# Performance work log

Measured on AMD Instinct MI355X. Metric: run time of the kernel, lower is better.

## Reference

```python
import jax, jax.numpy as jnp
import numpy as np

B, NMAX, H, DH, K = 16, 1024, 4, 32, 16
C = H * DH  # 128 = hidden_dim
T = 8192


def _dense_batch(feat, batch):
    # PyG to_dense_batch: [T, ...] + segment ids -> [B, NMAX, ...] + mask
    t = feat.shape[0]
    counts = jax.ops.segment_sum(jnp.ones((t,), jnp.int32), batch, num_segments=B)
    starts = jnp.concatenate([jnp.zeros((1,), jnp.int32), jnp.cumsum(counts)[:-1].astype(jnp.int32)])
    idx = jnp.arange(t) - starts[batch]
    dense = jnp.zeros((B, NMAX) + feat.shape[1:], feat.dtype).at[batch, idx].set(feat)
    mask = jnp.zeros((B, NMAX), bool).at[batch, idx].set(True)
    return dense, mask


def _forward(batch, x, pos, emb_W, emb_b, Wq, Wk, Wv0, Wv1, Wo0, Wo1, Wg, dist_scale, head_W, head_b):
    # 1) node embedding, then dense-batch (as in original forward)
    f0_flat = x @ emb_W + emb_b                      # [T, C]
    f0, mask = _dense_batch(f0_flat, batch)          # [B,N,C], [B,N]
    coords, _ = _dense_batch(pos, batch)             # [B,N,3]

    # 2) kNN graph from coordinates (num_neighbors=16, attend_self=True -> self is nearest)
    rel = coords[:, :, None, :] - coords[:, None, :, :]      # [B,N,N,3]
    d2 = jnp.sum(rel * rel, axis=-1)                         # [B,N,N]
    pv = mask[:, :, None] & mask[:, None, :]
    d2m = jnp.where(pv, d2, 1e9)
    _, nbr = jax.lax.top_k(-d2m, K)                          # [B,N,K]

    bidx = jnp.arange(B)[:, None, None]
    rel_n = jnp.take_along_axis(rel, nbr[..., None], axis=2)  # [B,N,K,3]
    d2_n = jnp.take_along_axis(d2, nbr, axis=2)               # [B,N,K]
    nbr_valid = jnp.take_along_axis(pv, nbr, axis=2)          # [B,N,K]
    dist = jnp.sqrt(d2_n + 1e-6)
    direc = rel_n / dist[..., None]                           # degree-1 spherical harmonic (unit rel dir)

    # 3) SE(3)-equivariant kNN attention (degree-0 and degree-1 outputs)
    q = (f0 @ Wq).reshape(B, NMAX, H, DH)
    k_n = (f0 @ Wk)[bidx, nbr].reshape(B, NMAX, K, H, DH)
    v0_n = (f0 @ Wv0)[bidx, nbr].reshape(B, NMAX, K, H, DH)
    v1_n = (f0 @ Wv1)[bidx, nbr].reshape(B, NMAX, K, H, DH)

    logits = jnp.einsum('bnhd,bnkhd->bnhk', q, k_n) / np.sqrt(DH)
    logits = logits - jax.nn.softplus(dist_scale)[None, None, :, None] * dist[:, :, None, :]
    logits = jnp.where(nbr_valid[:, :, None, :], logits, -1e9)
    attn = jax.nn.softmax(logits, axis=-1)                    # [B,N,H,K]

    out0 = jnp.einsum('bnhk,bnkhd->bnhd', attn, v0_n).reshape(B, NMAX, C)
    out1 = jnp.einsum('bnhk,bnkhd,bnkj->bnhdj', attn, v1_n, direc).reshape(B, NMAX, C, 3)

    # equivariant channel mixing of type-1, then invariant norm gates type-0 (residual)
    f1 = jnp.einsum('bncj,cd->bndj', out1, Wo1)               # [B,N,C,3]
    inv = jnp.sqrt(jnp.sum(f1 * f1, axis=-1) + 1e-6)          # [B,N,C]
    f0_out = f0 + out0 @ Wo0 + inv @ Wg

    # 4) masked mean pool over nodes + linear head
    mf = mask.astype(f0_out.dtype)
    pooled = jnp.sum(f0_out * mf[..., None], axis=1) / jnp.maximum(jnp.sum(mf, axis=1, keepdims=True), 1.0)
    return pooled @ head_W + head_b                           # [B, 19]


def setup_inputs() -> dict:
    key = jax.random.key(0)
    ks = jax.random.split(key, 16)
    def w(k, shape, fan_in):
        return jax.random.normal(k, shape, jnp.float32) / np.sqrt(fan_in)
    return {
        'x': jax.random.normal(ks[0], (T, 11), jnp.float32),
        'pos': jax.random.normal(ks[1], (T, 3), jnp.float32),
        'batch': jnp.sort(jax.random.randint(ks[2], (T,), 0, B)),
        'emb_W': w(ks[3], (11, C), 11), 'emb_b': jnp.zeros((C,), jnp.float32),
        'Wq': w(ks[4], (C, C), C), 'Wk': w(ks[5], (C, C), C),
        'Wv0': w(ks[6], (C, C), C), 'Wv1': w(ks[7], (C, C), C),
        'Wo0': w(ks[8], (C, C), C), 'Wo1': w(ks[9], (C, C), C),
        'Wg': w(ks[10], (C, C), C),
        'dist_scale': jax.random.normal(ks[11], (H,), jnp.float32) * 0.1,
        'head_W': w(ks[12], (C, 19), C), 'head_b': jnp.zeros((19,), jnp.float32),
    }


def reference(x, pos, batch, emb_W, emb_b, Wq, Wk, Wv0, Wv1, Wo0, Wo1, Wg, dist_scale, head_W, head_b):
    return _forward(batch, x, pos, emb_W, emb_b, Wq, Wk, Wv0, Wv1, Wo0, Wo1, Wg, dist_scale, head_W, head_b)
```

## Files before the change

### kernel.cpp

```cpp
#include <hip/hip_runtime.h>
#include <hip/hip_bf16.h>
#include <math.h>

#define T_NODES 8192
#define BGRAPHS 16
#define CDIM 128
#define HEADS 4
#define DHEAD 32
#define KNN 16

__device__ __forceinline__ void seg_probe(const int* __restrict__ batch, int t,
                                          int lane, int& s_out, int& n_out) {
    int b = batch[t];
    int pb = t - lane * 16;
    int qf = t + lane * 16;
    int vb = batch[pb < 0 ? 0 : pb];
    int vf = batch[qf > T_NODES - 1 ? T_NODES - 1 : qf];
    bool eqb = (pb >= 0) && (vb == b);
    bool eqf = (qf < T_NODES) && (vf == b);
    unsigned long long mb = __ballot(eqb);
    unsigned long long mf = __ballot(eqf);
    int m1 = (~mb == 0ULL) ? 64 : (int)__builtin_ctzll(~mb);
    int m2 = (~mf == 0ULL) ? 64 : (int)__builtin_ctzll(~mf);
    int wsb = (m1 == 64) ? (t - 1023) : (t - m1 * 16 + 1);
    int wsf = (m2 == 64) ? (t + 1009) : (t + (m2 - 1) * 16 + 1);
    int pos2 = (lane < 16) ? (wsb + lane) : (wsf + (lane - 16));
    int pc = pos2 < 0 ? 0 : (pos2 > T_NODES - 1 ? T_NODES - 1 : pos2);
    int v2 = batch[pc];
    bool cb = (lane < 16) && ((pos2 < 0) || (v2 < b));
    bool cf = (lane >= 16) && (lane < 32) && (pos2 < T_NODES) && (v2 == b);
    s_out = wsb + (int)__popcll(__ballot(cb));
    n_out = wsf + (int)__popcll(__ballot(cf)) - s_out;
}

template <int NS>
__device__ __forceinline__ void knn_body(const float* __restrict__ pos,
                                         int t, int s, int n, int lane,
                                         int* __restrict__ nbr,
                                         float4* __restrict__ dird) {
    float px = pos[t * 3 + 0], py = pos[t * 3 + 1], pz = pos[t * 3 + 2];
    float sd[NS];
    int ss[NS];
#pragma unroll
    for (int sl = 0; sl < NS; ++sl) {
        int j = lane + sl * 64;
        float d2 = 1e30f;
        if (j < n) {
            int jj = s + j;
            float dx = px - pos[jj * 3 + 0];
            float dy = py - pos[jj * 3 + 1];
            float dz = pz - pos[jj * 3 + 2];
            d2 = dx * dx + dy * dy + dz * dz;
        }
        sd[sl] = d2;
        ss[sl] = sl;
    }
#pragma unroll
    for (int p = 1; p < NS; p <<= 1) {
#pragma unroll
        for (int k = p; k >= 1; k >>= 1) {
#pragma unroll
            for (int j = (k & (p - 1)); j + k < NS; j += 2 * k) {
#pragma unroll
                for (int i = 0; i < k; ++i) {
                    if (i + j + k < NS && ((i + j) / (2 * p)) == ((i + j + k) / (2 * p))) {
                        int a = i + j, c2 = i + j + k;
                        bool sw = sd[a] > sd[c2];
                        float td = sd[a];
                        int ts = ss[a];
                        sd[a] = sw ? sd[c2] : sd[a];
                        ss[a] = sw ? ss[c2] : ss[a];
                        sd[c2] = sw ? td : sd[c2];
                        ss[c2] = sw ? ts : ss[c2];
                    }
                }
            }
        }
    }

    float resd = 1e30f;
    int resj = -1;
#pragma unroll
    for (int r = 0; r < KNN; ++r) {
        float rd = sd[0];
#pragma unroll
        for (int off = 32; off >= 1; off >>= 1) {
            rd = fminf(rd, __shfl_xor(rd, off));
        }
        unsigned long long mask = __ballot(sd[0] == rd);
        int wl = (int)__builtin_ctzll(mask);
        int ws = __shfl(ss[0], wl);
        if (lane == r) { resd = rd; resj = wl + ws * 64; }
        if (lane == wl) {
#pragma unroll
            for (int i = 0; i < NS - 1; ++i) { sd[i] = sd[i + 1]; ss[i] = ss[i + 1]; }
            sd[NS - 1] = 1e30f;
        }
    }

    if (lane < KNN) {
        bool valid = (resd < 1e29f);
        int jf = valid ? (s + resj) : -1;
        nbr[t * KNN + lane] = jf;
        float dd = sqrtf(resd + 1e-6f);
        float dx = 0.f, dy = 0.f, dz = 0.f;
        if (valid) {
            float inv = 1.f / dd;
            dx = (px - pos[jf * 3 + 0]) * inv;
            dy = (py - pos[jf * 3 + 1]) * inv;
            dz = (pz - pos[jf * 3 + 2]) * inv;
        }
        float4 v;
        v.x = dx; v.y = dy; v.z = dz; v.w = dd;
        dird[t * KNN + lane] = v;
    }
}

__device__ __forceinline__ bool knn_tau(const float* __restrict__ pos,
                                        int t, int s, int n, int lane,
                                        float* __restrict__ ldsD,
                                        int* __restrict__ ldsI,
                                        int* __restrict__ nbr,
                                        float4* __restrict__ dird) {
    const int NS = 18;
    int l32 = lane & 31;
    float px = pos[t * 3 + 0], py = pos[t * 3 + 1], pz = pos[t * 3 + 2];
    float sd[NS];
#pragma unroll
    for (int sl = 0; sl < NS; ++sl) {
        int j = l32 + sl * 32;
        float d2 = 1e30f;
        if (j < n) {
            int jj = s + j;
            float dx = px - pos[jj * 3 + 0];
            float dy = py - pos[jj * 3 + 1];
            float dz = pz - pos[jj * 3 + 2];
            d2 = dx * dx + dy * dy + dz * dz;
        }
        sd[sl] = d2;
    }
    float v = sd[0];
#pragma unroll
    for (int sl = 1; sl < NS; ++sl) v = fminf(v, sd[sl]);
#pragma unroll
    for (int k = 2; k <= 32; k <<= 1) {
#pragma unroll
        for (int j = k >> 1; j > 0; j >>= 1) {
            float o = __shfl_xor(v, j);
            bool up = ((l32 & k) == 0);
            bool lower = ((l32 & j) == 0);
            v = (lower == up) ? fminf(v, o) : fmaxf(v, o);
        }
    }
    float tau = __shfl(v, (lane & 32) + 15);

    int cnt = 0;
#pragma unroll
    for (int sl = 0; sl < NS; ++sl) cnt += (sd[sl] <= tau) ? 1 : 0;
    int pfx = cnt;
#pragma unroll
    for (int off = 1; off < 32; off <<= 1) {
        int y = __shfl(pfx, lane - off);
        if (l32 >= off) pfx += y;
    }
    int M = __shfl(pfx, (lane & 32) + 31);
    if (__ballot(M > 32)) return false;

    int wp = pfx - cnt;
    float* bd = ldsD + (lane >> 5) * 32;
    int* bi = ldsI + (lane >> 5) * 32;
#pragma unroll
    for (int sl = 0; sl < NS; ++sl) {
        if (sd[sl] <= tau) { bd[wp] = sd[sl]; bi[wp] = l32 + sl * 32; ++wp; }
    }
    __asm__ volatile("s_waitcnt lgkmcnt(0)" ::: "memory");

    float kd = (l32 < M) ? bd[l32] : 1e30f;
    int ki = (l32 < M) ? bi[l32] : 0;
#pragma unroll
    for (int k = 2; k <= 32; k <<= 1) {
#pragma unroll
        for (int j = k >> 1; j > 0; j >>= 1) {
            float od = __shfl_xor(kd, j);
            int oi = __shfl_xor(ki, j);
            bool up = ((l32 & k) == 0);
            bool lower = ((l32 & j) == 0);
            bool keepMin = (lower == up);
            bool take = keepMin ? (od < kd) : (od > kd);
            kd = keepMin ? fminf(kd, od) : fmaxf(kd, od);
            ki = take ? oi : ki;
        }
    }

    if (l32 < KNN) {
        bool valid = (kd < 1e29f);
        int jf = valid ? (s + ki) : -1;
        nbr[t * KNN + l32] = jf;
        float dd = sqrtf(kd + 1e-6f);
        float dx = 0.f, dy = 0.f, dz = 0.f;
        if (valid) {
            float inv = 1.f / dd;
            dx = (px - pos[jf * 3 + 0]) * inv;
            dy = (py - pos[jf * 3 + 1]) * inv;
            dz = (pz - pos[jf * 3 + 2]) * inv;
        }
        float4 vv;
        vv.x = dx; vv.y = dy; vv.z = dz; vv.w = dd;
        dird[t * KNN + l32] = vv;
    }
    return true;
}

__global__ __launch_bounds__(256) void k_par(const float* __restrict__ pos,
                                             const int* __restrict__ batch,
                                             const float* __restrict__ x,
                                             const float* __restrict__ embW,
                                             const float* __restrict__ embb,
                                             const float* __restrict__ Wq,
                                             const float* __restrict__ Wk,
                                             const float* __restrict__ Wv0,
                                             const float* __restrict__ Wv1,
                                             const float* __restrict__ Wo0,
                                             const float* __restrict__ Wg,
                                             const float* __restrict__ headW,
                                             int* __restrict__ nbr,
                                             float4* __restrict__ dird,
                                             float* __restrict__ qkvv,
                                             float* __restrict__ poolF0,
                                             float* __restrict__ H1,
                                             float* __restrict__ H2) {
    __shared__ float smem[CDIM * 20];
    int bid = blockIdx.x;
    int tid = threadIdx.x;

    if (bid >= 1536) {
        int m = bid - 1536;
        const float* W = m ? Wg : Wo0;
        float* H = m ? H2 : H1;
        for (int i = tid; i < CDIM * 19; i += 256) smem[i] = headW[i];
        __syncthreads();
        for (int i = tid; i < CDIM * 19; i += 256) {
            int c = i / 19, o = i - c * 19;
            float acc = 0.f;
#pragma unroll 8
            for (int d = 0; d < CDIM; ++d) acc += W[c * CDIM + d] * smem[d * 19 + o];
            H[i] = acc;
        }
        return;
    }

    int g = bid / 3, r = bid - g * 3;
    if (r == 2) {
        float (*sf)[CDIM] = (float (*)[CDIM])smem;
        int t0 = g * 16;
        {
            int col = tid & 127;
            int pr = tid >> 7;
            float ew[11];
#pragma unroll
            for (int i = 0; i < 11; ++i) ew[i] = embW[i * CDIM + col];
            float eb = embb[col];
            float acc_run = 0.f;
            int gprev = batch[t0 + pr * 8];
#pragma unroll
            for (int nn8 = 0; nn8 < 8; ++nn8) {
                int nn = pr * 8 + nn8;
                int t = t0 + nn;
                float acc = eb;
#pragma unroll
                for (int i = 0; i < 11; ++i) acc += x[t * 11 + i] * ew[i];
                sf[nn][col] = acc;
                int gb = batch[t];
                if (gb != gprev) {
                    atomicAdd(&poolF0[gprev * CDIM + col], acc_run);
                    acc_run = 0.f;
                    gprev = gb;
                }
                acc_run += acc;
            }
            atomicAdd(&poolF0[gprev * CDIM + col], acc_run);
        }
        __syncthreads();

        const float* W1 = (tid < 128) ? Wq : Wk;
        const float* W2 = (tid < 128) ? Wv0 : Wv1;
        int col = tid & 127;

        float acc1[16], acc2[16];
#pragma unroll
        for (int nn = 0; nn < 16; ++nn) { acc1[nn] = 0.f; acc2[nn] = 0.f; }

        for (int c0 = 0; c0 < CDIM; c0 += 8) {
            float w1[8], w2[8];
#pragma unroll
            for (int cc = 0; cc < 8; ++cc) {
                w1[cc] = W1[(c0 + cc) * CDIM + col];
                w2[cc] = W2[(c0 + cc) * CDIM + col];
            }
#pragma unroll
            for (int nn = 0; nn < 16; ++nn) {
                float4 fa = *(const float4*)&sf[nn][c0];
                float4 fb = *(const float4*)&sf[nn][c0 + 4];
                acc1[nn] += fa.x * w1[0] + fa.y * w1[1] + fa.z * w1[2] + fa.w * w1[3]
                          + fb.x * w1[4] + fb.y * w1[5] + fb.z * w1[6] + fb.w * w1[7];
                acc2[nn] += fa.x * w2[0] + fa.y * w2[1] + fa.z * w2[2] + fa.w * w2[3]
                          + fb.x * w2[4] + fb.y * w2[5] + fb.z * w2[6] + fb.w * w2[7];
            }
        }
#pragma unroll
        for (int nn = 0; nn < 16; ++nn) {
            qkvv[(size_t)(t0 + nn) * 512 + tid] = acc1[nn];
            qkvv[(size_t)(t0 + nn) * 512 + 256 + tid] = acc2[nn];
        }
        return;
    }

    int kidx = g * 2 + r;
    int wave = tid >> 6;
    int lane = tid & 63;
    int tA = kidx * 8 + wave * 2;
    int tB = tA + 1;

    int sA, nA, sB, nB;
    seg_probe(batch, tA, lane, sA, nA);
    seg_probe(batch, tB, lane, sB, nB);

    float* ldsD = smem + wave * 64;
    int* ldsI = (int*)(smem + 256) + wave * 64;

    int nmax = nA > nB ? nA : nB;
    bool done = false;
    if (nmax <= 576) {
        int t = (lane < 32) ? tA : tB;
        int s = (lane < 32) ? sA : sB;
        int n = (lane < 32) ? nA : nB;
        done = knn_tau(pos, t, s, n, lane, ldsD, ldsI, nbr, dird);
    }
    if (!done) {
        knn_body<16>(pos, tA, sA, nA, lane, nbr, dird);
        knn_body<16>(pos, tB, sB, nB, lane, nbr, dird);
    }
}

__global__ __launch_bounds__(256) void k_attn(const float* __restrict__ qkvv,
                                              const int* __restrict__ nbr,
                                              const float4* __restrict__ dird,
                                              const int* __restrict__ batch,
                                              const float* __restrict__ dist_scale,
                                              const float* __restrict__ Wo1,
                                              float* __restrict__ poolO0,
                                              float* __restrict__ poolInv) {
    __shared__ float  s_a[4][64];
    __shared__ float4 s_d[4][16];
    __shared__ int    s_j[4][16];
    __shared__ float  s_o1[4][CDIM][4];
    __shared__ float  s_part[CDIM][13];
    __shared__ int    s_gid[4];

    int bid = blockIdx.x;
    int swz = (bid & 7) * (T_NODES / 32) + (bid >> 3);
    int wave = threadIdx.x >> 6;
    int lane = threadIdx.x & 63;
    int t0 = swz * 4;
    int t = t0 + wave;

    if (threadIdx.x < 4) s_gid[threadIdx.x] = batch[t0 + threadIdx.x];

    int k = lane & 15;
    int h = lane >> 4;

    int j = nbr[t * KNN + k];
    float4 dv = dird[t * KNN + k];
    if (h == 0) { s_j[wave][k] = j; s_d[wave][k] = dv; }

    const float4* qv = (const float4*)&qkvv[(size_t)t * 512 + h * DHEAD];
    const float4* kv = (j >= 0) ? (const float4*)&qkvv[(size_t)j * 512 + 128 + h * DHEAD] : qv;
    float dot = 0.f;
#pragma unroll
    for (int i = 0; i < 8; ++i) {
        float4 a = qv[i], b2 = kv[i];
        dot += a.x * b2.x + a.y * b2.y + a.z * b2.z + a.w * b2.w;
    }
    float xs = dist_scale[h];
    float sp = (xs > 20.f) ? xs : log1pf(expf(xs));
    float lg = (j >= 0) ? (dot * 0.17677669529663687f - sp * dv.w) : -1e30f;

    float m = lg;
    m = fmaxf(m, __shfl_xor(m, 1));
    m = fmaxf(m, __shfl_xor(m, 2));
    m = fmaxf(m, __shfl_xor(m, 4));
    m = fmaxf(m, __shfl_xor(m, 8));
    float e = expf(lg - m);
    float ssum = e;
    ssum += __shfl_xor(ssum, 1);
    ssum += __shfl_xor(ssum, 2);
    ssum += __shfl_xor(ssum, 4);
    ssum += __shfl_xor(ssum, 8);
    s_a[wave][h * 16 + k] = e / ssum;

    __syncthreads();

    int c2 = lane * 2;
    int hh = lane >> 4;

    float o0x = 0.f, o0y = 0.f;
    float o1xx = 0.f, o1xy = 0.f;
    float o1yx = 0.f, o1yy = 0.f;
    float o1zx = 0.f, o1zy = 0.f;

#pragma unroll
    for (int kk = 0; kk < KNN; ++kk) {
        int jj = s_j[wave][kk];
        if (jj >= 0) {
            float a = s_a[wave][hh * 16 + kk];
            float4 d = s_d[wave][kk];
            float2 v0 = *(const float2*)&qkvv[(size_t)jj * 512 + 256 + c2];
            float2 v1 = *(const float2*)&qkvv[(size_t)jj * 512 + 384 + c2];
            o0x += a * v0.x;
            o0y += a * v0.y;
            float w1x = a * v1.x, w1y = a * v1.y;
            o1xx += w1x * d.x; o1xy += w1y * d.x;
            o1yx += w1x * d.y; o1yy += w1y * d.y;
            o1zx += w1x * d.z; o1zy += w1y * d.z;
        }
    }

    {
        float4 w0; w0.x = o1xx; w0.y = o1yx; w0.z = o1zx; w0.w = o0x;
        float4 w1; w1.x = o1xy; w1.y = o1yy; w1.z = o1zy; w1.w = o0y;
        *(float4*)&s_o1[wave][c2][0] = w0;
        *(float4*)&s_o1[wave][c2 + 1][0] = w1;
    }
    __syncthreads();

    int d = threadIdx.x & 127;
    int half = threadIdx.x >> 7;

    float acc[4][3];
#pragma unroll
    for (int nn = 0; nn < 4; ++nn) { acc[nn][0] = 0.f; acc[nn][1] = 0.f; acc[nn][2] = 0.f; }

    int cb0 = half * 64;
#pragma unroll 4
    for (int c = cb0; c < cb0 + 64; ++c) {
        float wv = Wo1[c * CDIM + d];
#pragma unroll
        for (int nn = 0; nn < 4; ++nn) {
            float4 v = *(const float4*)&s_o1[nn][c][0];
            acc[nn][0] += v.x * wv;
            acc[nn][1] += v.y * wv;
            acc[nn][2] += v.z * wv;
        }
    }
    if (half == 1) {
#pragma unroll
        for (int nn = 0; nn < 4; ++nn) {
            s_part[d][nn * 3 + 0] = acc[nn][0];
            s_part[d][nn * 3 + 1] = acc[nn][1];
            s_part[d][nn * 3 + 2] = acc[nn][2];
        }
    }
    __syncthreads();
    if (half == 0) {
        float accO = 0.f, accI = 0.f;
        int gprev = s_gid[0];
#pragma unroll
        for (int nn = 0; nn < 4; ++nn) {
            float fx = acc[nn][0] + s_part[d][nn * 3 + 0];
            float fy = acc[nn][1] + s_part[d][nn * 3 + 1];
            float fz = acc[nn][2] + s_part[d][nn * 3 + 2];
            float iv = sqrtf(fx * fx + fy * fy + fz * fz + 1e-6f);
            float o0v = s_o1[nn][d][3];
            int gb = s_gid[nn];
            if (gb != gprev) {
                atomicAdd(&poolO0[gprev * CDIM + d], accO);
                atomicAdd(&poolInv[gprev * CDIM + d], accI);
                accO = 0.f; accI = 0.f;
                gprev = gb;
            }
            accO += o0v;
            accI += iv;
        }
        atomicAdd(&poolO0[gprev * CDIM + d], accO);
        atomicAdd(&poolInv[gprev * CDIM + d], accI);
    }
}

__global__ __launch_bounds__(640) void k_pool(const float* __restrict__ poolF0,
                                              const float* __restrict__ poolO0,
                                              const float* __restrict__ poolInv,
                                              const int* __restrict__ batch,
                                              const float* __restrict__ headW,
                                              const float* __restrict__ H1,
                                              const float* __restrict__ H2,
                                              const float* __restrict__ headb,
                                              float* __restrict__ out) {
    __shared__ float P0[CDIM], P1[CDIM], P2[CDIM];
    int b = blockIdx.x;
    int tid = threadIdx.x;

    int lo = 0, hi = T_NODES;
    while (lo < hi) {
        int mid = (lo + hi) >> 1;
        bool lt = batch[mid] < b;
        lo = lt ? mid + 1 : lo;
        hi = lt ? hi : mid;
    }
    int s = lo;
    lo = 0; hi = T_NODES;
    while (lo < hi) {
        int mid = (lo + hi) >> 1;
        bool le = batch[mid] <= b;
        lo = le ? mid + 1 : lo;
        hi = le ? hi : mid;
    }
    int n = lo - s;
    float inv_n = 1.f / fmaxf((float)n, 1.f);

    if (tid < CDIM) {
        P0[tid] = poolF0[b * CDIM + tid] * inv_n;
        P1[tid] = poolO0[b * CDIM + tid] * inv_n;
        P2[tid] = poolInv[b * CDIM + tid] * inv_n;
    }
    __syncthreads();

    if (tid < 19 * 32) {
        int o = tid >> 5;
        int l = tid & 31;
        float p = 0.f;
#pragma unroll
        for (int cc = 0; cc < 4; ++cc) {
            int ch = l + cc * 32;
            p += P0[ch] * headW[ch * 19 + o]
               + P1[ch] * H1[ch * 19 + o]
               + P2[ch] * H2[ch * 19 + o];
        }
        p += __shfl_xor(p, 16);
        p += __shfl_xor(p, 8);
        p += __shfl_xor(p, 4);
        p += __shfl_xor(p, 2);
        p += __shfl_xor(p, 1);
        if (l == 0) out[b * 19 + o] = p + headb[o];
    }
}

extern "C" void kernel_launch(void* const* d_in, const int* in_sizes, int n_in,
                              void* d_out, int out_size, void* d_ws, size_t ws_size,
                              hipStream_t stream) {
    const float* x    = (const float*)d_in[0];
    const float* pos  = (const float*)d_in[1];
    const int* batch  = (const int*)d_in[2];
    const float* embW = (const float*)d_in[3];
    const float* embb = (const float*)d_in[4];
    const float* Wq   = (const float*)d_in[5];
    const float* Wk   = (const float*)d_in[6];
    const float* Wv0  = (const float*)d_in[7];
    const float* Wv1  = (const float*)d_in[8];
    const float* Wo0  = (const float*)d_in[9];
    const float* Wo1  = (const float*)d_in[10];
    const float* Wg   = (const float*)d_in[11];
    const float* dist_scale = (const float*)d_in[12];
    const float* headW = (const float*)d_in[13];
    const float* headb = (const float*)d_in[14];
    float* out = (float*)d_out;

    char* w = (char*)d_ws;
    float* qkvv = (float*)(w + 256);
    int* nbr    = (int*)(qkvv + (size_t)T_NODES * 512);
    float4* dird = (float4*)(nbr + (size_t)T_NODES * KNN);
    float* poolF0 = (float*)(dird + (size_t)T_NODES * KNN);
    float* poolO0 = poolF0 + BGRAPHS * CDIM;
    float* poolInv = poolO0 + BGRAPHS * CDIM;
    float* H1   = poolInv + BGRAPHS * CDIM;
    float* H2   = H1 + CDIM * 19;

    hipMemsetAsync(poolF0, 0, 3 * BGRAPHS * CDIM * sizeof(float), stream);
    k_par<<<1538, 256, 0, stream>>>(pos, batch, x, embW, embb, Wq, Wk, Wv0, Wv1,
                                    Wo0, Wg, headW, nbr, dird, qkvv, poolF0, H1, H2);
    k_attn<<<T_NODES / 4, 256, 0, stream>>>(qkvv, nbr, dird, batch, dist_scale, Wo1,
                                            poolO0, poolInv);
    k_pool<<<BGRAPHS, 640, 0, stream>>>(poolF0, poolO0, poolInv, batch, headW,
                                        H1, H2, headb, out);
}
```

Baseline: 112.2 us.

## Use atomic work queues to dynamically schedule kNN and projection tasks

Replaces the static block-to-task mapping in the fused kNN/projection kernel with two global atomic counters, one per task type. Each block pulls tasks in a loop, and odd and even blocks prefer different queues. The projection task is halved to 8 nodes, which doubles the task count and halves the accumulator registers. The aim is to balance uneven kNN work across CUs, at the cost of per-task atomics, extra barriers and twice as many weight-matrix reloads.

New measurement: 171.7 us. 53.0% more time.

```diff
diff --git a/kernel.cpp b/kernel.cpp
--- a/kernel.cpp
+++ b/kernel.cpp
@@ -223,6 +223,7 @@
                                              const float* __restrict__ Wo0,
                                              const float* __restrict__ Wg,
                                              const float* __restrict__ headW,
+                                             int* __restrict__ qcnt,
                                              int* __restrict__ nbr,
                                              float4* __restrict__ dird,
                                              float* __restrict__ qkvv,
@@ -230,11 +231,13 @@
                                              float* __restrict__ H1,
                                              float* __restrict__ H2) {
     __shared__ float smem[CDIM * 20];
+    __shared__ int smemi[256];
+    __shared__ int s_task;
     int bid = blockIdx.x;
     int tid = threadIdx.x;
 
-    if (bid >= 1536) {
-        int m = bid - 1536;
+    if (bid >= 2048) {
+        int m = bid - 2048;
         const float* W = m ? Wg : Wo0;
         float* H = m ? H2 : H1;
         for (int i = tid; i < CDIM * 19; i += 256) smem[i] = headW[i];
@@ -249,96 +252,124 @@
         return;
     }
 
-    int g = bid / 3, r = bid - g * 3;
-    if (r == 2) {
-        float (*sf)[CDIM] = (float (*)[CDIM])smem;
-        int t0 = g * 16;
-        {
+    bool preferA = (bid & 1) != 0;
+    int* qA = qcnt;
+    int* qB = qcnt + 1;
+
+    for (;;) {
+        if (tid == 0) {
+            int task = -1;
+            if (preferA) {
+                int i = atomicAdd(qA, 1);
+                if (i < 1024) task = i;
+                else {
+                    int jq = atomicAdd(qB, 1);
+                    if (jq < 1024) task = 1024 + jq;
+                }
+            } else {
+                int jq = atomicAdd(qB, 1);
+                if (jq < 1024) task = 1024 + jq;
+                else {
+                    int i = atomicAdd(qA, 1);
+                    if (i < 1024) task = i;
+                }
+            }
+            s_task = task;
+        }
+        __syncthreads();
+        int task = s_task;
+        __syncthreads();
+        if (task < 0) break;
+
+        if (task < 1024) {
+            int wave = tid >> 6;
+            int lane = tid & 63;
+            int tA = task * 8 + wave * 2;
+            int tB = tA + 1;
+
+            int sA, nA, sB, nB;
+            seg_probe(batch, tA, lane, sA, nA);
+            seg_probe(batch, tB, lane, sB, nB);
+
+            float* ldsD = smem + wave * 64;
+            int* ldsI = smemi + wave * 64;
+
+            int nmax = nA > nB ? nA : nB;
+            bool done = false;
+            if (nmax <= 576) {
+                int t = (lane < 32) ? tA : tB;
+                int s = (lane < 32) ? sA : sB;
+                int n = (lane < 32) ? nA : nB;
+                done = knn_tau(pos, t, s, n, lane, ldsD, ldsI, nbr, dird);
+            }
+            if (!done) {
+                knn_body<16>(pos, tA, sA, nA, lane, nbr, dird);
+                knn_body<16>(pos, tB, sB, nB, lane, nbr, dird);
+            }
+        } else {
+            float (*sf)[CDIM] = (float (*)[CDIM])smem;
+            int t0 = (task - 1024) * 8;
+            {
+                int col = tid & 127;
+                int pr = tid >> 7;
+                float ew[11];
+#pragma unroll
+                for (int i = 0; i < 11; ++i) ew[i] = embW[i * CDIM + col];
+                float eb = embb[col];
+                float acc_run = 0.f;
+                int gprev = batch[t0 + pr * 4];
+#pragma unroll
+                for (int nn4 = 0; nn4 < 4; ++nn4) {
+                    int nn = pr * 4 + nn4;
+                    int t = t0 + nn;
+                    float acc = eb;
+#pragma unroll
+                    for (int i = 0; i < 11; ++i) acc += x[t * 11 + i] * ew[i];
+                    sf[nn][col] = acc;
+                    int gb = batch[t];
+                    if (gb != gprev) {
+                        atomicAdd(&poolF0[gprev * CDIM + col], acc_run);
+                        acc_run = 0.f;
+                        gprev = gb;
+                    }
+                    acc_run += acc;
+                }
+                atomicAdd(&poolF0[gprev * CDIM + col], acc_run);
+            }
+            __syncthreads();
+
+            const float* W1 = (tid < 128) ? Wq : Wk;
+            const float* W2 = (tid < 128) ? Wv0 : Wv1;
             int col = tid & 127;
-            int pr = tid >> 7;
-            float ew[11];
-#pragma unroll
-            for (int i = 0; i < 11; ++i) ew[i] = embW[i * CDIM + col];
-            float eb = embb[col];
-            float acc_run = 0.f;
-            int gprev = batch[t0 + pr * 8];
-#pragma unroll
-            for (int nn8 = 0; nn8 < 8; ++nn8) {
-                int nn = pr * 8 + nn8;
-                int t = t0 + nn;
-                float acc = eb;
-#pragma unroll
-                for (int i = 0; i < 11; ++i) acc += x[t * 11 + i] * ew[i];
-                sf[nn][col] = acc;
-                int gb = batch[t];
-                if (gb != gprev) {
-                    atomicAdd(&poolF0[gprev * CDIM + col], acc_run);
-                    acc_run = 0.f;
-                    gprev = gb;
+
+            float acc1[8], acc2[8];
+#pragma unroll
+            for (int nn = 0; nn < 8; ++nn) { acc1[nn] = 0.f; acc2[nn] = 0.f; }
+
+            for (int c0 = 0; c0 < CDIM; c0 += 8) {
+                float w1[8], w2[8];
+#pragma unroll
+                for (int cc = 0; cc < 8; ++cc) {
+                    w1[cc] = W1[(c0 + cc) * CDIM + col];
+                    w2[cc] = W2[(c0 + cc) * CDIM + col];
                 }
-                acc_run += acc;
-            }
-            atomicAdd(&poolF0[gprev * CDIM + col], acc_run);
+#pragma unroll
+                for (int nn = 0; nn < 8; ++nn) {
+                    float4 fa = *(const float4*)&sf[nn][c0];
+                    float4 fb = *(const float4*)&sf[nn][c0 + 4];
+                    acc1[nn] += fa.x * w1[0] + fa.y * w1[1] + fa.z * w1[2] + fa.w * w1[3]
+                              + fb.x * w1[4] + fb.y * w1[5] + fb.z * w1[6] + fb.w * w1[7];
+                    acc2[nn] += fa.x * w2[0] + fa.y * w2[1] + fa.z * w2[2] + fa.w * w2[3]
+                              + fb.x * w2[4] + fb.y * w2[5] + fb.z * w2[6] + fb.w * w2[7];
+                }
+            }
+#pragma unroll
+            for (int nn = 0; nn < 8; ++nn) {
+                qkvv[(size_t)(t0 + nn) * 512 + tid] = acc1[nn];
+                qkvv[(size_t)(t0 + nn) * 512 + 256 + tid] = acc2[nn];
+            }
         }
         __syncthreads();
-
-        const float* W1 = (tid < 128) ? Wq : Wk;
-        const float* W2 = (tid < 128) ? Wv0 : Wv1;
-        int col = tid & 127;
-
-        float acc1[16], acc2[16];
-#pragma unroll
-        for (int nn = 0; nn < 16; ++nn) { acc1[nn] = 0.f; acc2[nn] = 0.f; }
-
-        for (int c0 = 0; c0 < CDIM; c0 += 8) {
-            float w1[8], w2[8];
-#pragma unroll
-            for (int cc = 0; cc < 8; ++cc) {
-                w1[cc] = W1[(c0 + cc) * CDIM + col];
-                w2[cc] = W2[(c0 + cc) * CDIM + col];
-            }
-#pragma unroll
-            for (int nn = 0; nn < 16; ++nn) {
-                float4 fa = *(const float4*)&sf[nn][c0];
-                float4 fb = *(const float4*)&sf[nn][c0 + 4];
-                acc1[nn] += fa.x * w1[0] + fa.y * w1[1] + fa.z * w1[2] + fa.w * w1[3]
-                          + fb.x * w1[4] + fb.y * w1[5] + fb.z * w1[6] + fb.w * w1[7];
-                acc2[nn] += fa.x * w2[0] + fa.y * w2[1] + fa.z * w2[2] + fa.w * w2[3]
-                          + fb.x * w2[4] + fb.y * w2[5] + fb.z * w2[6] + fb.w * w2[7];
-            }
-        }
-#pragma unroll
-        for (int nn = 0; nn < 16; ++nn) {
-            qkvv[(size_t)(t0 + nn) * 512 + tid] = acc1[nn];
-            qkvv[(size_t)(t0 + nn) * 512 + 256 + tid] = acc2[nn];
-        }
-        return;
-    }
-
-    int kidx = g * 2 + r;
-    int wave = tid >> 6;
-    int lane = tid & 63;
-    int tA = kidx * 8 + wave * 2;
-    int tB = tA + 1;
-
-    int sA, nA, sB, nB;
-    seg_probe(batch, tA, lane, sA, nA);
-    seg_probe(batch, tB, lane, sB, nB);
-
-    float* ldsD = smem + wave * 64;
-    int* ldsI = (int*)(smem + 256) + wave * 64;
-
-    int nmax = nA > nB ? nA : nB;
-    bool done = false;
-    if (nmax <= 576) {
-        int t = (lane < 32) ? tA : tB;
-        int s = (lane < 32) ? sA : sB;
-        int n = (lane < 32) ? nA : nB;
-        done = knn_tau(pos, t, s, n, lane, ldsD, ldsI, nbr, dird);
-    }
-    if (!done) {
-        knn_body<16>(pos, tA, sA, nA, lane, nbr, dird);
-        knn_body<16>(pos, tB, sB, nB, lane, nbr, dird);
     }
 }
 
@@ -571,12 +602,13 @@
     float* poolF0 = (float*)(dird + (size_t)T_NODES * KNN);
     float* poolO0 = poolF0 + BGRAPHS * CDIM;
     float* poolInv = poolO0 + BGRAPHS * CDIM;
-    float* H1   = poolInv + BGRAPHS * CDIM;
+    int* qcnt  = (int*)(poolInv + BGRAPHS * CDIM);
+    float* H1   = (float*)(qcnt + 16);
     float* H2   = H1 + CDIM * 19;
 
-    hipMemsetAsync(poolF0, 0, 3 * BGRAPHS * CDIM * sizeof(float), stream);
-    k_par<<<1538, 256, 0, stream>>>(pos, batch, x, embW, embb, Wq, Wk, Wv0, Wv1,
-                                    Wo0, Wg, headW, nbr, dird, qkvv, poolF0, H1, H2);
+    hipMemsetAsync(poolF0, 0, 3 * BGRAPHS * CDIM * sizeof(float) + 16 * sizeof(int), stream);
+    k_par<<<2050, 256, 0, stream>>>(pos, batch, x, embW, embb, Wq, Wk, Wv0, Wv1,
+                                    Wo0, Wg, headW, qcnt, nbr, dird, qkvv, poolF0, H1, H2);
     k_attn<<<T_NODES / 4, 256, 0, stream>>>(qkvv, nbr, dird, batch, dist_scale, Wo1,
                                             poolO0, poolInv);
     k_pool<<<BGRAPHS, 640, 0, stream>>>(poolF0, poolO0, poolInv, batch, headW,
```
